# Kernel optimization log

Hardware: AMD Instinct MI355X
Metric: run time of the kernel (lower is better)

The kernel has to match this reference:

```python
import jax, jax.numpy as jnp
import numpy as np

EPS = 1e-5

def _bn_relu(z, gamma, beta):
    # BatchNorm1d (training mode: biased batch stats) + ReLU, per-feature over batch dim
    mean = jnp.mean(z, axis=0)
    var = jnp.var(z, axis=0)  # biased, matches torch BN normalization
    zn = (z - mean) * jax.lax.rsqrt(var + EPS) * gamma + beta
    return jax.nn.relu(zn)


def setup_inputs() -> dict:
    key = jax.random.key(0)
    ks = jax.random.split(key, 16)
    N, D_IN, H, D_OUT = 2097152, 16, 32, 1
    def lin(kw, kb, fan_in, fan_out):
        bound = 1.0 / np.sqrt(fan_in)
        W = jax.random.uniform(kw, (fan_out, fan_in), jnp.float32, -bound, bound)
        b = jax.random.uniform(kb, (fan_out,), jnp.float32, -bound, bound)
        return W, b
    W1, b1 = lin(ks[0], ks[1], D_IN, H)
    W2, b2 = lin(ks[2], ks[3], H, H)
    W3, b3 = lin(ks[4], ks[5], H, H)
    W4, b4 = lin(ks[6], ks[7], H, D_OUT)
    x = jax.random.normal(ks[8], (N, D_IN), jnp.float32)
    return {
        "x": x,
        "W1": W1, "b1": b1, "g1": jnp.ones((H,), jnp.float32), "be1": jnp.zeros((H,), jnp.float32),
        "W2": W2, "b2": b2, "g2": jnp.ones((H,), jnp.float32), "be2": jnp.zeros((H,), jnp.float32),
        "W3": W3, "b3": b3, "g3": jnp.ones((H,), jnp.float32), "be3": jnp.zeros((H,), jnp.float32),
        "W4": W4, "b4": b4,
    }


def reference(x, W1, b1, g1, be1, W2, b2, g2, be2, W3, b3, g3, be3, W4, b4):
    p1 = _bn_relu(x @ W1.T + b1, g1, be1)    # [N, H]
    p2 = _bn_relu(p1 @ W2.T + b2, g2, be2)   # [N, H]
    p3 = _bn_relu(p2 @ W3.T + b3, g3, be3)   # [N, H]
    return p3 @ W4.T + b4                    # [N, 1]
```

## Files before the change

kernel.cpp:

```cpp
#include <hip/hip_runtime.h>

#define EPS 1e-5f
#define NTHR 256
#define NBLK 1024
#define NSLOT 8

typedef __bf16 bf16x8 __attribute__((ext_vector_type(8)));
typedef float f32x16 __attribute__((ext_vector_type(16)));


template<int DEPTH>
__global__ __launch_bounds__(NTHR) void k_fwd(
    const float* __restrict__ x,
    const float* __restrict__ W1, const float* __restrict__ b1,
    const float* __restrict__ g1, const float* __restrict__ be1,
    const float* __restrict__ W2, const float* __restrict__ b2,
    const float* __restrict__ g2, const float* __restrict__ be2,
    const float* __restrict__ W3, const float* __restrict__ b3,
    const float* __restrict__ g3, const float* __restrict__ be3,
    const float* __restrict__ W4, const float* __restrict__ b4,
    float* __restrict__ ws, float* __restrict__ out, int N)
{
    constexpr bool STATS = (DEPTH < 4);
    __shared__ float s_stat[3][64];
    __shared__ float s_a[3][32];
    __shared__ float s_e[3][32];
    __shared__ float s_b[64];

    const int tid = threadIdx.x;
    const float invN = 1.0f / (float)N;

    if (tid < 64) {
        for (int L = 0; L < DEPTH - 1; ++L) {
            float a = 0.f;
            #pragma unroll
            for (int s = 0; s < NSLOT; ++s) a += ws[L * (NSLOT * 64) + s * 64 + tid];
            s_stat[L][tid] = a;
        }
    }
    __syncthreads();
    if (tid < 32) {
        const float* gs[3]  = {g1, g2, g3};
        const float* bes[3] = {be1, be2, be3};
        const float* bs[3]  = {b1, b2, b3};
        for (int L = 0; L < DEPTH - 1; ++L) {
            float mu = s_stat[L][tid] * invN;
            float v  = s_stat[L][32 + tid] * invN - mu * mu;
            float a  = gs[L][tid] * rsqrtf(v + EPS);
            s_a[L][tid] = a;
            s_e[L][tid] = bs[L][tid] - mu + bes[L][tid] / a;
        }
    }
    if (STATS && tid < 64) s_b[tid] = 0.f;
    __syncthreads();

    const int lane = tid & 63;
    const int h = lane >> 5;
    const int ml = lane & 31;

    bf16x8 w1f;
    {
        const float* p = W1 + ml * 16 + h * 8;
        #pragma unroll
        for (int j = 0; j < 8; ++j) w1f[j] = (__bf16)p[j];
    }
    bf16x8 w2f0 = {}, w2f1 = {}, w3f0 = {}, w3f1 = {};
    if (DEPTH >= 2) {
        #pragma unroll
        for (int kh = 0; kh < 2; ++kh)
            #pragma unroll
            for (int j = 0; j < 8; ++j) {
                int pk = (j & 3) + 8 * (j >> 2) + 4 * h + 16 * kh;
                float v = W2[ml * 32 + pk] * s_a[0][pk];
                if (kh == 0) w2f0[j] = (__bf16)v; else w2f1[j] = (__bf16)v;
            }
    }
    if (DEPTH >= 3) {
        #pragma unroll
        for (int kh = 0; kh < 2; ++kh)
            #pragma unroll
            for (int j = 0; j < 8; ++j) {
                int pk = (j & 3) + 8 * (j >> 2) + 4 * h + 16 * kh;
                float v = W3[ml * 32 + pk] * s_a[1][pk];
                if (kh == 0) w3f0[j] = (__bf16)v; else w3f1[j] = (__bf16)v;
            }
    }

    f32x16 c1, c2 = {}, c3 = {};
    float w4c[16];
    #pragma unroll
    for (int i = 0; i < 16; ++i) {
        int p = (i & 3) + 8 * (i >> 2) + 4 * h;
        c1[i] = (DEPTH == 1) ? b1[p] : s_e[0][p];
        if (DEPTH >= 2) c2[i] = (DEPTH == 2) ? b2[p] : s_e[1][p];
        if (DEPTH >= 3) c3[i] = (DEPTH == 3) ? b3[p] : s_e[2][p];
        if (DEPTH == 4) w4c[i] = W4[p] * s_a[2][p]; else w4c[i] = 0.f;
    }
    float b4v = (DEPTH == 4) ? b4[0] : 0.f;

    const int ntiles = N >> 5;
    const int nwaves = gridDim.x * (NTHR / 64);
    const int gwave  = blockIdx.x * (NTHR / 64) + (tid >> 6);

    float sums[16], sqs[16];
    #pragma unroll
    for (int i = 0; i < 16; ++i) { sums[i] = 0.f; sqs[i] = 0.f; }

    for (int t = gwave; t < ntiles; t += nwaves) {
        int row = (t << 5) + ml;
        const float4* xp = (const float4*)(x + (size_t)row * 16 + h * 8);
        float4 u0 = xp[0], u1 = xp[1];
        bf16x8 xf;
        xf[0] = (__bf16)u0.x; xf[1] = (__bf16)u0.y; xf[2] = (__bf16)u0.z; xf[3] = (__bf16)u0.w;
        xf[4] = (__bf16)u1.x; xf[5] = (__bf16)u1.y; xf[6] = (__bf16)u1.z; xf[7] = (__bf16)u1.w;

        f32x16 a1 = __builtin_amdgcn_mfma_f32_32x32x16_bf16(w1f, xf, c1, 0, 0, 0);
        if (DEPTH == 1) {
            #pragma unroll
            for (int i = 0; i < 16; ++i) { sums[i] += a1[i]; sqs[i] = fmaf(a1[i], a1[i], sqs[i]); }
            continue;
        }
        bf16x8 qa, qb;
        #pragma unroll
        for (int j = 0; j < 8; ++j) {
            qa[j] = (__bf16)fmaxf(a1[j], 0.f);
            qb[j] = (__bf16)fmaxf(a1[8 + j], 0.f);
        }
        f32x16 a2 = __builtin_amdgcn_mfma_f32_32x32x16_bf16(w2f0, qa, c2, 0, 0, 0);
        a2 = __builtin_amdgcn_mfma_f32_32x32x16_bf16(w2f1, qb, a2, 0, 0, 0);
        if (DEPTH == 2) {
            #pragma unroll
            for (int i = 0; i < 16; ++i) { sums[i] += a2[i]; sqs[i] = fmaf(a2[i], a2[i], sqs[i]); }
            continue;
        }
        bf16x8 pa, pb;
        #pragma unroll
        for (int j = 0; j < 8; ++j) {
            pa[j] = (__bf16)fmaxf(a2[j], 0.f);
            pb[j] = (__bf16)fmaxf(a2[8 + j], 0.f);
        }
        f32x16 a3 = __builtin_amdgcn_mfma_f32_32x32x16_bf16(w3f0, pa, c3, 0, 0, 0);
        a3 = __builtin_amdgcn_mfma_f32_32x32x16_bf16(w3f1, pb, a3, 0, 0, 0);
        if (DEPTH == 3) {
            #pragma unroll
            for (int i = 0; i < 16; ++i) { sums[i] += a3[i]; sqs[i] = fmaf(a3[i], a3[i], sqs[i]); }
            continue;
        }
        float o = 0.f;
        #pragma unroll
        for (int i = 0; i < 16; ++i) o = fmaf(w4c[i], fmaxf(a3[i], 0.f), o);
        o += __shfl_xor(o, 32);
        if (h == 0) out[row] = o + b4v;
    }

    if (STATS) {
        #pragma unroll
        for (int i = 0; i < 16; ++i) {
            float s = sums[i], q = sqs[i];
            #pragma unroll
            for (int d = 1; d <= 16; d <<= 1) {
                s += __shfl_xor(s, d);
                q += __shfl_xor(q, d);
            }
            if (ml == 0) {
                int p = (i & 3) + 8 * (i >> 2) + 4 * h;
                atomicAdd(&s_b[p], s);
                atomicAdd(&s_b[32 + p], q);
            }
        }
        __syncthreads();
        if (tid < 64) {
            int L = DEPTH - 1;
            atomicAdd(&ws[L * (NSLOT * 64) + (blockIdx.x & (NSLOT - 1)) * 64 + tid], s_b[tid]);
        }
    }
}

extern "C" void kernel_launch(void* const* d_in, const int* in_sizes, int n_in,
                              void* d_out, int out_size, void* d_ws, size_t ws_size,
                              hipStream_t stream) {
    const float* x   = (const float*)d_in[0];
    const float* W1  = (const float*)d_in[1];
    const float* b1  = (const float*)d_in[2];
    const float* g1  = (const float*)d_in[3];
    const float* be1 = (const float*)d_in[4];
    const float* W2  = (const float*)d_in[5];
    const float* b2  = (const float*)d_in[6];
    const float* g2  = (const float*)d_in[7];
    const float* be2 = (const float*)d_in[8];
    const float* W3  = (const float*)d_in[9];
    const float* b3  = (const float*)d_in[10];
    const float* g3  = (const float*)d_in[11];
    const float* be3 = (const float*)d_in[12];
    const float* W4  = (const float*)d_in[13];
    const float* b4  = (const float*)d_in[14];
    float* out = (float*)d_out;
    float* ws  = (float*)d_ws;
    int N = in_sizes[0] / 16;

    hipMemsetAsync(ws, 0, 3 * NSLOT * 64 * sizeof(float), stream);

    k_fwd<1><<<NBLK, NTHR, 0, stream>>>(x, W1, b1, g1, be1, W2, b2, g2, be2, W3, b3, g3, be3, W4, b4, ws, out, N);
    k_fwd<2><<<NBLK, NTHR, 0, stream>>>(x, W1, b1, g1, be1, W2, b2, g2, be2, W3, b3, g3, be3, W4, b4, ws, out, N);
    k_fwd<3><<<NBLK, NTHR, 0, stream>>>(x, W1, b1, g1, be1, W2, b2, g2, be2, W3, b3, g3, be3, W4, b4, ws, out, N);
    k_fwd<4><<<NBLK, NTHR, 0, stream>>>(x, W1, b1, g1, be1, W2, b2, g2, be2, W3, b3, g3, be3, W4, b4, ws, out, N);
}
```

Measured before the change: 335.6 us.

## Cache bf16 MFMA-ready copy of x in workspace and unroll tile loop by two

```diff
diff --git a/kernel.cpp b/kernel.cpp
--- a/kernel.cpp
+++ b/kernel.cpp
@@ -11,7 +11,7 @@
 
 template<int DEPTH>
 __global__ __launch_bounds__(NTHR) void k_fwd(
-    const float* __restrict__ x,
+    const float* __restrict__ x, __bf16* __restrict__ xb,
     const float* __restrict__ W1, const float* __restrict__ b1,
     const float* __restrict__ g1, const float* __restrict__ be1,
     const float* __restrict__ W2, const float* __restrict__ b2,
@@ -19,7 +19,7 @@
     const float* __restrict__ W3, const float* __restrict__ b3,
     const float* __restrict__ g3, const float* __restrict__ be3,
     const float* __restrict__ W4, const float* __restrict__ b4,
-    float* __restrict__ ws, float* __restrict__ out, int N)
+    float* __restrict__ stats, float* __restrict__ out, int N)
 {
     constexpr bool STATS = (DEPTH < 4);
     __shared__ float s_stat[3][64];
@@ -34,7 +34,7 @@
         for (int L = 0; L < DEPTH - 1; ++L) {
             float a = 0.f;
             #pragma unroll
-            for (int s = 0; s < NSLOT; ++s) a += ws[L * (NSLOT * 64) + s * 64 + tid];
+            for (int s = 0; s < NSLOT; ++s) a += stats[L * (NSLOT * 64) + s * 64 + tid];
             s_stat[L][tid] = a;
         }
     }
@@ -96,7 +96,7 @@
         if (DEPTH >= 3) c3[i] = (DEPTH == 3) ? b3[p] : s_e[2][p];
         if (DEPTH == 4) w4c[i] = W4[p] * s_a[2][p]; else w4c[i] = 0.f;
     }
-    float b4v = (DEPTH == 4) ? b4[0] : 0.f;
+    const float b4v = (DEPTH == 4) ? b4[0] : 0.f;
 
     const int ntiles = N >> 5;
     const int nwaves = gridDim.x * (NTHR / 64);
@@ -106,19 +106,27 @@
     #pragma unroll
     for (int i = 0; i < 16; ++i) { sums[i] = 0.f; sqs[i] = 0.f; }
 
-    for (int t = gwave; t < ntiles; t += nwaves) {
-        int row = (t << 5) + ml;
-        const float4* xp = (const float4*)(x + (size_t)row * 16 + h * 8);
-        float4 u0 = xp[0], u1 = xp[1];
-        bf16x8 xf;
-        xf[0] = (__bf16)u0.x; xf[1] = (__bf16)u0.y; xf[2] = (__bf16)u0.z; xf[3] = (__bf16)u0.w;
-        xf[4] = (__bf16)u1.x; xf[5] = (__bf16)u1.y; xf[6] = (__bf16)u1.z; xf[7] = (__bf16)u1.w;
-
+    auto loadx = [&](int t) -> bf16x8 {
+        if (DEPTH == 1) {
+            int row = (t << 5) + ml;
+            const float4* xp = (const float4*)(x + (size_t)row * 16 + h * 8);
+            float4 u0 = xp[0], u1 = xp[1];
+            bf16x8 xf;
+            xf[0] = (__bf16)u0.x; xf[1] = (__bf16)u0.y; xf[2] = (__bf16)u0.z; xf[3] = (__bf16)u0.w;
+            xf[4] = (__bf16)u1.x; xf[5] = (__bf16)u1.y; xf[6] = (__bf16)u1.z; xf[7] = (__bf16)u1.w;
+            *(bf16x8*)(xb + ((size_t)t * 64 + lane) * 8) = xf;
+            return xf;
+        } else {
+            return *(const bf16x8*)(xb + ((size_t)t * 64 + lane) * 8);
+        }
+    };
+
+    auto tile = [&](int t, bf16x8 xf) {
         f32x16 a1 = __builtin_amdgcn_mfma_f32_32x32x16_bf16(w1f, xf, c1, 0, 0, 0);
         if (DEPTH == 1) {
             #pragma unroll
             for (int i = 0; i < 16; ++i) { sums[i] += a1[i]; sqs[i] = fmaf(a1[i], a1[i], sqs[i]); }
-            continue;
+            return;
         }
         bf16x8 qa, qb;
         #pragma unroll
@@ -131,7 +139,7 @@
         if (DEPTH == 2) {
             #pragma unroll
             for (int i = 0; i < 16; ++i) { sums[i] += a2[i]; sqs[i] = fmaf(a2[i], a2[i], sqs[i]); }
-            continue;
+            return;
         }
         bf16x8 pa, pb;
         #pragma unroll
@@ -144,13 +152,25 @@
         if (DEPTH == 3) {
             #pragma unroll
             for (int i = 0; i < 16; ++i) { sums[i] += a3[i]; sqs[i] = fmaf(a3[i], a3[i], sqs[i]); }
-            continue;
+            return;
         }
         float o = 0.f;
         #pragma unroll
         for (int i = 0; i < 16; ++i) o = fmaf(w4c[i], fmaxf(a3[i], 0.f), o);
         o += __shfl_xor(o, 32);
-        if (h == 0) out[row] = o + b4v;
+        if (h == 0) out[(t << 5) + ml] = o + b4v;
+    };
+
+    int t = gwave;
+    for (; t + nwaves < ntiles; t += 2 * nwaves) {
+        bf16x8 x0 = loadx(t);
+        bf16x8 x1 = loadx(t + nwaves);
+        tile(t, x0);
+        tile(t + nwaves, x1);
+    }
+    if (t < ntiles) {
+        bf16x8 x0 = loadx(t);
+        tile(t, x0);
     }
 
     if (STATS) {
@@ -171,7 +191,7 @@
         __syncthreads();
         if (tid < 64) {
             int L = DEPTH - 1;
-            atomicAdd(&ws[L * (NSLOT * 64) + (blockIdx.x & (NSLOT - 1)) * 64 + tid], s_b[tid]);
+            atomicAdd(&stats[L * (NSLOT * 64) + (blockIdx.x & (NSLOT - 1)) * 64 + tid], s_b[tid]);
         }
     }
 }
@@ -195,13 +215,15 @@
     const float* W4  = (const float*)d_in[13];
     const float* b4  = (const float*)d_in[14];
     float* out = (float*)d_out;
-    float* ws  = (float*)d_ws;
     int N = in_sizes[0] / 16;
 
-    hipMemsetAsync(ws, 0, 3 * NSLOT * 64 * sizeof(float), stream);
-
-    k_fwd<1><<<NBLK, NTHR, 0, stream>>>(x, W1, b1, g1, be1, W2, b2, g2, be2, W3, b3, g3, be3, W4, b4, ws, out, N);
-    k_fwd<2><<<NBLK, NTHR, 0, stream>>>(x, W1, b1, g1, be1, W2, b2, g2, be2, W3, b3, g3, be3, W4, b4, ws, out, N);
-    k_fwd<3><<<NBLK, NTHR, 0, stream>>>(x, W1, b1, g1, be1, W2, b2, g2, be2, W3, b3, g3, be3, W4, b4, ws, out, N);
-    k_fwd<4><<<NBLK, NTHR, 0, stream>>>(x, W1, b1, g1, be1, W2, b2, g2, be2, W3, b3, g3, be3, W4, b4, ws, out, N);
+    __bf16* xb   = (__bf16*)d_ws;
+    float* stats = (float*)((char*)d_ws + (size_t)N * 16 * 2);
+
+    hipMemsetAsync(stats, 0, 3 * NSLOT * 64 * sizeof(float), stream);
+
+    k_fwd<1><<<NBLK, NTHR, 0, stream>>>(x, xb, W1, b1, g1, be1, W2, b2, g2, be2, W3, b3, g3, be3, W4, b4, stats, out, N);
+    k_fwd<2><<<NBLK, NTHR, 0, stream>>>(x, xb, W1, b1, g1, be1, W2, b2, g2, be2, W3, b3, g3, be3, W4, b4, stats, out, N);
+    k_fwd<3><<<NBLK, NTHR, 0, stream>>>(x, xb, W1, b1, g1, be1, W2, b2, g2, be2, W3, b3, g3, be3, W4, b4, stats, out, N);
+    k_fwd<4><<<NBLK, NTHR, 0, stream>>>(x, xb, W1, b1, g1, be1, W2, b2, g2, be2, W3, b3, g3, be3, W4, b4, stats, out, N);
 }
```

Result: faster. 323.7 us (-3.6%).

## Fuse four passes into one persistent kernel with grid barriers and bf16 x cache

Applied to the files above, without the earlier changes.

```diff
diff --git a/kernel.cpp b/kernel.cpp
--- a/kernel.cpp
+++ b/kernel.cpp
@@ -2,16 +2,26 @@
 
 #define EPS 1e-5f
 #define NTHR 256
-#define NBLK 1024
-#define NSLOT 8
+#define NBLK 512
 
 typedef __bf16 bf16x8 __attribute__((ext_vector_type(8)));
 typedef float f32x16 __attribute__((ext_vector_type(16)));
 
 
-template<int DEPTH>
-__global__ __launch_bounds__(NTHR) void k_fwd(
-    const float* __restrict__ x,
+__device__ __forceinline__ void gbarrier(unsigned* cnt, unsigned target, int tid) {
+    __syncthreads();
+    __threadfence();
+    if (tid == 0) {
+        __hip_atomic_fetch_add(cnt, 1u, __ATOMIC_ACQ_REL, __HIP_MEMORY_SCOPE_AGENT);
+        while (__hip_atomic_load(cnt, __ATOMIC_ACQUIRE, __HIP_MEMORY_SCOPE_AGENT) < target)
+            __builtin_amdgcn_s_sleep(8);
+    }
+    __syncthreads();
+    __threadfence();
+}
+
+__global__ __launch_bounds__(NTHR, 2) void k_all(
+    const float* __restrict__ x, __bf16* __restrict__ xb,
     const float* __restrict__ W1, const float* __restrict__ b1,
     const float* __restrict__ g1, const float* __restrict__ be1,
     const float* __restrict__ W2, const float* __restrict__ b2,
@@ -19,107 +29,120 @@
     const float* __restrict__ W3, const float* __restrict__ b3,
     const float* __restrict__ g3, const float* __restrict__ be3,
     const float* __restrict__ W4, const float* __restrict__ b4,
-    float* __restrict__ ws, float* __restrict__ out, int N)
+    float* __restrict__ stats, unsigned* __restrict__ cnt,
+    float* __restrict__ out, int N)
 {
-    constexpr bool STATS = (DEPTH < 4);
-    __shared__ float s_stat[3][64];
-    __shared__ float s_a[3][32];
-    __shared__ float s_e[3][32];
-    __shared__ float s_b[64];
-
-    const int tid = threadIdx.x;
+    __shared__ float s_a[32], s_e[32], s_b[64];
+
+    const int tid  = threadIdx.x;
+    const int lane = tid & 63;
+    const int h    = lane >> 5;
+    const int ml   = lane & 31;
     const float invN = 1.0f / (float)N;
 
-    if (tid < 64) {
-        for (int L = 0; L < DEPTH - 1; ++L) {
-            float a = 0.f;
+    const int ntiles = N >> 5;
+    const int nwaves = NBLK * (NTHR / 64);
+    const int gwave  = blockIdx.x * (NTHR / 64) + (tid >> 6);
+
+    float sums[16], sqs[16];
+
+    auto zero_acc = [&]() {
+        #pragma unroll
+        for (int i = 0; i < 16; ++i) { sums[i] = 0.f; sqs[i] = 0.f; }
+    };
+    auto accum = [&](const f32x16& a) {
+        #pragma unroll
+        for (int i = 0; i < 16; ++i) { sums[i] += a[i]; sqs[i] = fmaf(a[i], a[i], sqs[i]); }
+    };
+    auto flush = [&](int L) {
+        __syncthreads();
+        if (tid < 64) s_b[tid] = 0.f;
+        __syncthreads();
+        #pragma unroll
+        for (int i = 0; i < 16; ++i) {
+            float s = sums[i], q = sqs[i];
             #pragma unroll
-            for (int s = 0; s < NSLOT; ++s) a += ws[L * (NSLOT * 64) + s * 64 + tid];
-            s_stat[L][tid] = a;
-        }
-    }
-    __syncthreads();
-    if (tid < 32) {
-        const float* gs[3]  = {g1, g2, g3};
-        const float* bes[3] = {be1, be2, be3};
-        const float* bs[3]  = {b1, b2, b3};
-        for (int L = 0; L < DEPTH - 1; ++L) {
-            float mu = s_stat[L][tid] * invN;
-            float v  = s_stat[L][32 + tid] * invN - mu * mu;
-            float a  = gs[L][tid] * rsqrtf(v + EPS);
-            s_a[L][tid] = a;
-            s_e[L][tid] = bs[L][tid] - mu + bes[L][tid] / a;
-        }
-    }
-    if (STATS && tid < 64) s_b[tid] = 0.f;
-    __syncthreads();
-
-    const int lane = tid & 63;
-    const int h = lane >> 5;
-    const int ml = lane & 31;
-
-    bf16x8 w1f;
-    {
-        const float* p = W1 + ml * 16 + h * 8;
-        #pragma unroll
-        for (int j = 0; j < 8; ++j) w1f[j] = (__bf16)p[j];
-    }
-    bf16x8 w2f0 = {}, w2f1 = {}, w3f0 = {}, w3f1 = {};
-    if (DEPTH >= 2) {
+            for (int d = 1; d <= 16; d <<= 1) { s += __shfl_xor(s, d); q += __shfl_xor(q, d); }
+            if (ml == 0) {
+                int p = (i & 3) + 8 * (i >> 2) + 4 * h;
+                atomicAdd(&s_b[p], s);
+                atomicAdd(&s_b[32 + p], q);
+            }
+        }
+        __syncthreads();
+        if (tid < 64) atomicAdd(&stats[L * 64 + tid], s_b[tid]);
+    };
+    auto derive = [&](int L, const float* g, const float* be, const float* b) {
+        if (tid < 32) {
+            float su = __hip_atomic_load(&stats[L * 64 + tid], __ATOMIC_RELAXED, __HIP_MEMORY_SCOPE_AGENT);
+            float sq = __hip_atomic_load(&stats[L * 64 + 32 + tid], __ATOMIC_RELAXED, __HIP_MEMORY_SCOPE_AGENT);
+            float mu = su * invN;
+            float v  = sq * invN - mu * mu;
+            float a  = g[tid] * rsqrtf(v + EPS);
+            s_a[tid] = a;
+            s_e[tid] = b[tid] - mu + be[tid] / a;
+        }
+        __syncthreads();
+    };
+    auto run2 = [&](auto&& body) {
+        int t = gwave;
+        for (; t + nwaves < ntiles; t += 2 * nwaves) { body(t); body(t + nwaves); }
+        if (t < ntiles) body(t);
+    };
+    auto loadxb = [&](int t) -> bf16x8 {
+        return *(const bf16x8*)(xb + ((size_t)t * 64 + lane) * 8);
+    };
+    auto build_wf = [&](const float* W, bf16x8& f0, bf16x8& f1) {
         #pragma unroll
         for (int kh = 0; kh < 2; ++kh)
             #pragma unroll
             for (int j = 0; j < 8; ++j) {
                 int pk = (j & 3) + 8 * (j >> 2) + 4 * h + 16 * kh;
-                float v = W2[ml * 32 + pk] * s_a[0][pk];
-                if (kh == 0) w2f0[j] = (__bf16)v; else w2f1[j] = (__bf16)v;
+                float v = W[ml * 32 + pk] * s_a[pk];
+                if (kh == 0) f0[j] = (__bf16)v; else f1[j] = (__bf16)v;
             }
-    }
-    if (DEPTH >= 3) {
-        #pragma unroll
-        for (int kh = 0; kh < 2; ++kh)
-            #pragma unroll
-            for (int j = 0; j < 8; ++j) {
-                int pk = (j & 3) + 8 * (j >> 2) + 4 * h + 16 * kh;
-                float v = W3[ml * 32 + pk] * s_a[1][pk];
-                if (kh == 0) w3f0[j] = (__bf16)v; else w3f1[j] = (__bf16)v;
-            }
-    }
-
-    f32x16 c1, c2 = {}, c3 = {};
-    float w4c[16];
-    #pragma unroll
-    for (int i = 0; i < 16; ++i) {
-        int p = (i & 3) + 8 * (i >> 2) + 4 * h;
-        c1[i] = (DEPTH == 1) ? b1[p] : s_e[0][p];
-        if (DEPTH >= 2) c2[i] = (DEPTH == 2) ? b2[p] : s_e[1][p];
-        if (DEPTH >= 3) c3[i] = (DEPTH == 3) ? b3[p] : s_e[2][p];
-        if (DEPTH == 4) w4c[i] = W4[p] * s_a[2][p]; else w4c[i] = 0.f;
-    }
-    float b4v = (DEPTH == 4) ? b4[0] : 0.f;
-
-    const int ntiles = N >> 5;
-    const int nwaves = gridDim.x * (NTHR / 64);
-    const int gwave  = blockIdx.x * (NTHR / 64) + (tid >> 6);
-
-    float sums[16], sqs[16];
-    #pragma unroll
-    for (int i = 0; i < 16; ++i) { sums[i] = 0.f; sqs[i] = 0.f; }
-
-    for (int t = gwave; t < ntiles; t += nwaves) {
+    };
+
+    bf16x8 w1f;
+    {
+        const float* p = W1 + ml * 16 + h * 8;
+        #pragma unroll
+        for (int j = 0; j < 8; ++j) w1f[j] = (__bf16)p[j];
+    }
+    f32x16 c1;
+    #pragma unroll
+    for (int i = 0; i < 16; ++i) c1[i] = b1[(i & 3) + 8 * (i >> 2) + 4 * h];
+
+    zero_acc();
+    run2([&](int t) {
         int row = (t << 5) + ml;
         const float4* xp = (const float4*)(x + (size_t)row * 16 + h * 8);
         float4 u0 = xp[0], u1 = xp[1];
         bf16x8 xf;
         xf[0] = (__bf16)u0.x; xf[1] = (__bf16)u0.y; xf[2] = (__bf16)u0.z; xf[3] = (__bf16)u0.w;
         xf[4] = (__bf16)u1.x; xf[5] = (__bf16)u1.y; xf[6] = (__bf16)u1.z; xf[7] = (__bf16)u1.w;
-
-        f32x16 a1 = __builtin_amdgcn_mfma_f32_32x32x16_bf16(w1f, xf, c1, 0, 0, 0);
-        if (DEPTH == 1) {
-            #pragma unroll
-            for (int i = 0; i < 16; ++i) { sums[i] += a1[i]; sqs[i] = fmaf(a1[i], a1[i], sqs[i]); }
-            continue;
-        }
+        *(bf16x8*)(xb + ((size_t)t * 64 + lane) * 8) = xf;
+        f32x16 a1 = __builtin_amdgcn_mfma_f32_32x32x16_bf16(w1f, xf, c1, 0, 0, 0);
+        accum(a1);
+    });
+    flush(0);
+    gbarrier(cnt, NBLK, tid);
+    derive(0, g1, be1, b1);
+
+    bf16x8 w2f0, w2f1;
+    build_wf(W2, w2f0, w2f1);
+    f32x16 c2;
+    #pragma unroll
+    for (int i = 0; i < 16; ++i) {
+        int p = (i & 3) + 8 * (i >> 2) + 4 * h;
+        c1[i] = s_e[p];
+        c2[i] = b2[p];
+    }
+
+    zero_acc();
+    run2([&](int t) {
+        bf16x8 xf = loadxb(t);
+        f32x16 a1 = __builtin_amdgcn_mfma_f32_32x32x16_bf16(w1f, xf, c1, 0, 0, 0);
         bf16x8 qa, qb;
         #pragma unroll
         for (int j = 0; j < 8; ++j) {
@@ -128,11 +151,34 @@
         }
         f32x16 a2 = __builtin_amdgcn_mfma_f32_32x32x16_bf16(w2f0, qa, c2, 0, 0, 0);
         a2 = __builtin_amdgcn_mfma_f32_32x32x16_bf16(w2f1, qb, a2, 0, 0, 0);
-        if (DEPTH == 2) {
-            #pragma unroll
-            for (int i = 0; i < 16; ++i) { sums[i] += a2[i]; sqs[i] = fmaf(a2[i], a2[i], sqs[i]); }
-            continue;
-        }
+        accum(a2);
+    });
+    flush(1);
+    gbarrier(cnt, 2 * NBLK, tid);
+    derive(1, g2, be2, b2);
+
+    bf16x8 w3f0, w3f1;
+    build_wf(W3, w3f0, w3f1);
+    f32x16 c3;
+    #pragma unroll
+    for (int i = 0; i < 16; ++i) {
+        int p = (i & 3) + 8 * (i >> 2) + 4 * h;
+        c2[i] = s_e[p];
+        c3[i] = b3[p];
+    }
+
+    zero_acc();
+    run2([&](int t) {
+        bf16x8 xf = loadxb(t);
+        f32x16 a1 = __builtin_amdgcn_mfma_f32_32x32x16_bf16(w1f, xf, c1, 0, 0, 0);
+        bf16x8 qa, qb;
+        #pragma unroll
+        for (int j = 0; j < 8; ++j) {
+            qa[j] = (__bf16)fmaxf(a1[j], 0.f);
+            qb[j] = (__bf16)fmaxf(a1[8 + j], 0.f);
+        }
+        f32x16 a2 = __builtin_amdgcn_mfma_f32_32x32x16_bf16(w2f0, qa, c2, 0, 0, 0);
+        a2 = __builtin_amdgcn_mfma_f32_32x32x16_bf16(w2f1, qb, a2, 0, 0, 0);
         bf16x8 pa, pb;
         #pragma unroll
         for (int j = 0; j < 8; ++j) {
@@ -141,39 +187,46 @@
         }
         f32x16 a3 = __builtin_amdgcn_mfma_f32_32x32x16_bf16(w3f0, pa, c3, 0, 0, 0);
         a3 = __builtin_amdgcn_mfma_f32_32x32x16_bf16(w3f1, pb, a3, 0, 0, 0);
-        if (DEPTH == 3) {
-            #pragma unroll
-            for (int i = 0; i < 16; ++i) { sums[i] += a3[i]; sqs[i] = fmaf(a3[i], a3[i], sqs[i]); }
-            continue;
-        }
+        accum(a3);
+    });
+    flush(2);
+    gbarrier(cnt, 3 * NBLK, tid);
+    derive(2, g3, be3, b3);
+
+    float w4c[16];
+    #pragma unroll
+    for (int i = 0; i < 16; ++i) {
+        int p = (i & 3) + 8 * (i >> 2) + 4 * h;
+        c3[i]  = s_e[p];
+        w4c[i] = W4[p] * s_a[p];
+    }
+    const float b4v = b4[0];
+
+    run2([&](int t) {
+        bf16x8 xf = loadxb(t);
+        f32x16 a1 = __builtin_amdgcn_mfma_f32_32x32x16_bf16(w1f, xf, c1, 0, 0, 0);
+        bf16x8 qa, qb;
+        #pragma unroll
+        for (int j = 0; j < 8; ++j) {
+            qa[j] = (__bf16)fmaxf(a1[j], 0.f);
+            qb[j] = (__bf16)fmaxf(a1[8 + j], 0.f);
+        }
+        f32x16 a2 = __builtin_amdgcn_mfma_f32_32x32x16_bf16(w2f0, qa, c2, 0, 0, 0);
+        a2 = __builtin_amdgcn_mfma_f32_32x32x16_bf16(w2f1, qb, a2, 0, 0, 0);
+        bf16x8 pa, pb;
+        #pragma unroll
+        for (int j = 0; j < 8; ++j) {
+            pa[j] = (__bf16)fmaxf(a2[j], 0.f);
+            pb[j] = (__bf16)fmaxf(a2[8 + j], 0.f);
+        }
+        f32x16 a3 = __builtin_amdgcn_mfma_f32_32x32x16_bf16(w3f0, pa, c3, 0, 0, 0);
+        a3 = __builtin_amdgcn_mfma_f32_32x32x16_bf16(w3f1, pb, a3, 0, 0, 0);
         float o = 0.f;
         #pragma unroll
         for (int i = 0; i < 16; ++i) o = fmaf(w4c[i], fmaxf(a3[i], 0.f), o);
         o += __shfl_xor(o, 32);
-        if (h == 0) out[row] = o + b4v;
-    }
-
-    if (STATS) {
-        #pragma unroll
-        for (int i = 0; i < 16; ++i) {
-            float s = sums[i], q = sqs[i];
-            #pragma unroll
-            for (int d = 1; d <= 16; d <<= 1) {
-                s += __shfl_xor(s, d);
-                q += __shfl_xor(q, d);
-            }
-            if (ml == 0) {
-                int p = (i & 3) + 8 * (i >> 2) + 4 * h;
-                atomicAdd(&s_b[p], s);
-                atomicAdd(&s_b[32 + p], q);
-            }
-        }
-        __syncthreads();
-        if (tid < 64) {
-            int L = DEPTH - 1;
-            atomicAdd(&ws[L * (NSLOT * 64) + (blockIdx.x & (NSLOT - 1)) * 64 + tid], s_b[tid]);
-        }
-    }
+        if (h == 0) out[(t << 5) + ml] = o + b4v;
+    });
 }
 
 extern "C" void kernel_launch(void* const* d_in, const int* in_sizes, int n_in,
@@ -195,13 +248,15 @@
     const float* W4  = (const float*)d_in[13];
     const float* b4  = (const float*)d_in[14];
     float* out = (float*)d_out;
-    float* ws  = (float*)d_ws;
     int N = in_sizes[0] / 16;
 
-    hipMemsetAsync(ws, 0, 3 * NSLOT * 64 * sizeof(float), stream);
-
-    k_fwd<1><<<NBLK, NTHR, 0, stream>>>(x, W1, b1, g1, be1, W2, b2, g2, be2, W3, b3, g3, be3, W4, b4, ws, out, N);
-    k_fwd<2><<<NBLK, NTHR, 0, stream>>>(x, W1, b1, g1, be1, W2, b2, g2, be2, W3, b3, g3, be3, W4, b4, ws, out, N);
-    k_fwd<3><<<NBLK, NTHR, 0, stream>>>(x, W1, b1, g1, be1, W2, b2, g2, be2, W3, b3, g3, be3, W4, b4, ws, out, N);
-    k_fwd<4><<<NBLK, NTHR, 0, stream>>>(x, W1, b1, g1, be1, W2, b2, g2, be2, W3, b3, g3, be3, W4, b4, ws, out, N);
+    __bf16* xb   = (__bf16*)d_ws;
+    char* ctrl   = (char*)d_ws + (size_t)N * 32;
+    float* stats = (float*)ctrl;
+    unsigned* cnt = (unsigned*)(ctrl + 192 * sizeof(float));
+
+    hipMemsetAsync(ctrl, 0, 1024, stream);
+
+    k_all<<<NBLK, NTHR, 0, stream>>>(x, xb, W1, b1, g1, be1, W2, b2, g2, be2,
+                                     W3, b3, g3, be3, W4, b4, stats, cnt, out, N);
 }
```

Measured after the change: 566.3 us. 1.69x slower.
